# Optimization experiments

Measured on AMD Instinct MI355X. Metric: run time of the kernel, lower is better.

Reference implementation:

```python
import jax, jax.numpy as jnp
import numpy as np

B, T, C, H = 4, 2048, 512, 8
HS = C // H  # head_size = 64
EPS = 1e-5


def layernorm(x, g, b):
    mu = jnp.mean(x, axis=-1, keepdims=True)
    var = jnp.mean(jnp.square(x - mu), axis=-1, keepdims=True)
    return (x - mu) * jax.lax.rsqrt(var + EPS) * g + b


def setup_inputs() -> dict:
    key = jax.random.key(0)
    ks = jax.random.split(key, 12)
    s_attn = 1.0 / np.sqrt(C)
    s_ff1 = 1.0 / np.sqrt(C)
    s_ff2 = 1.0 / np.sqrt(4 * C)
    return {
        "x": jax.random.normal(ks[0], (B, T, C), jnp.float32),
        "wq": jax.random.normal(ks[1], (H, C, HS), jnp.float32) * s_attn,
        "wk": jax.random.normal(ks[2], (H, C, HS), jnp.float32) * s_attn,
        "wv": jax.random.normal(ks[3], (H, C, HS), jnp.float32) * s_attn,
        "w1": jax.random.normal(ks[4], (C, 4 * C), jnp.float32) * s_ff1,
        "b1": jnp.zeros((4 * C,), jnp.float32),
        "w2": jax.random.normal(ks[5], (4 * C, C), jnp.float32) * s_ff2,
        "b2": jnp.zeros((C,), jnp.float32),
        "ln1_g": jnp.ones((C,), jnp.float32),
        "ln1_b": jnp.zeros((C,), jnp.float32),
        "ln2_g": jnp.ones((C,), jnp.float32),
        "ln2_b": jnp.zeros((C,), jnp.float32),
    }


def reference(x, wq, wk, wv, w1, b1, w2, b2, ln1_g, ln1_b, ln2_g, ln2_b):
    # pre-LN multi-head causal self-attention
    h = layernorm(x, ln1_g, ln1_b)                       # [B,T,C]
    q = jnp.einsum("btc,hcd->bhtd", h, wq)
    k = jnp.einsum("btc,hcd->bhtd", h, wk)
    v = jnp.einsum("btc,hcd->bhtd", h, wv)
    # NOTE: source scales by full embed dim C, not head_size
    scores = jnp.einsum("bhtd,bhsd->bhts", q, k) * (C ** -0.5)  # [B,H,T,T]
    causal = jnp.tril(jnp.ones((T, T), bool))
    scores = jnp.where(causal, scores, -jnp.inf)
    att = jax.nn.softmax(scores, axis=-1)
    out = jnp.einsum("bhts,bhsd->bhtd", att, v)          # [B,H,T,HS]
    out = out.transpose(0, 2, 1, 3).reshape(B, T, C)     # concat heads
    x = x + out
    # FFN with residual
    h2 = layernorm(x, ln2_g, ln2_b)
    ff = jax.nn.relu(h2 @ w1 + b1) @ w2 + b2
    return x + ff
```

## Files before the change

kernel.cpp:

```cpp
#include <hip/hip_runtime.h>

typedef unsigned short ushort_t;
typedef __attribute__((ext_vector_type(8))) short short8;
typedef __attribute__((ext_vector_type(4))) float floatx4;

#define B_  4
#define T_  2048
#define C_  512
#define H_  8
#define HS_ 64
#define M_  (B_*T_)
#define SCALE2 0.06376140168547404f

__device__ __forceinline__ float b2f(ushort_t u) {
  union { unsigned int i; float f; } w; w.i = ((unsigned int)u) << 16; return w.f;
}
__device__ __forceinline__ ushort_t f2b(float f) {
  union { float f; unsigned int i; } w; w.f = f;
  unsigned int x = w.i;
  return (ushort_t)((x + 0x7fffu + ((x >> 16) & 1u)) >> 16);
}
__device__ __forceinline__ unsigned int cvtpk(float a, float b) {
  unsigned int r;
  asm("v_cvt_pk_bf16_f32 %0, %1, %2" : "=v"(r) : "v"(a), "v"(b));
  return r;
}
__device__ __forceinline__ void gl_lds16(const ushort_t* g, ushort_t* l) {
  __builtin_amdgcn_global_load_lds((const unsigned int*)g, (unsigned int*)l, 16, 0, 0);
}

__global__ __launch_bounds__(256) void transpose_all(const float* __restrict__ wq,
                                                     const float* __restrict__ wk,
                                                     const float* __restrict__ wv,
                                                     const float* __restrict__ w1,
                                                     const float* __restrict__ w2,
                                                     ushort_t* __restrict__ qkvt,
                                                     ushort_t* __restrict__ w1t,
                                                     ushort_t* __restrict__ w2t) {
  __shared__ ushort_t t[32][33];
  int idx = blockIdx.x;
  const float* in; ushort_t* out; int K, N, bx, by, z = 0;
  float scl = (idx < 256) ? SCALE2 : 1.0f;
  if (idx < 768) {
    int seg = idx >> 8, li = idx & 255;
    in = seg == 0 ? wq : (seg == 1 ? wk : wv);
    out = qkvt + (size_t)seg * 262144;
    K = 512; N = 64;
    z = li >> 5; li &= 31;
    bx = li & 1; by = li >> 1;
  } else if (idx < 1792) {
    int li = idx - 768;
    in = w1; out = w1t; K = 512; N = 2048;
    bx = li & 63; by = li >> 6;
  } else {
    int li = idx - 1792;
    in = w2; out = w2t; K = 2048; N = 512;
    bx = li & 15; by = li >> 4;
  }
  size_t zoff = (size_t)z * K * N;
  int n0 = bx * 32, k0 = by * 32;
  int tx = threadIdx.x & 31, ty = threadIdx.x >> 5;
#pragma unroll
  for (int i = 0; i < 4; i++)
    t[ty + 8 * i][tx] = f2b(in[zoff + (size_t)(k0 + ty + 8 * i) * N + n0 + tx] * scl);
  __syncthreads();
#pragma unroll
  for (int i = 0; i < 4; i++)
    out[zoff + (size_t)(n0 + ty + 8 * i) * K + k0 + tx] = t[tx][ty + 8 * i];
}

__global__ __launch_bounds__(256) void ln_k(const float* __restrict__ X,
                                            const float* __restrict__ g,
                                            const float* __restrict__ bb,
                                            ushort_t* __restrict__ Y) {
  int wave = threadIdx.x >> 6, lane = threadIdx.x & 63;
  size_t row = (size_t)blockIdx.x * 4 + wave;
  float v[8], s = 0.f, s2 = 0.f;
#pragma unroll
  for (int i = 0; i < 8; i++) {
    float x = X[row * C_ + lane + 64 * i];
    v[i] = x; s += x; s2 += x * x;
  }
#pragma unroll
  for (int off = 32; off >= 1; off >>= 1) {
    s += __shfl_xor(s, off); s2 += __shfl_xor(s2, off);
  }
  float mu = s * (1.0f / C_);
  float var = s2 * (1.0f / C_) - mu * mu;
  float rs = rsqrtf(var + 1e-5f);
  ushort_t* yr = Y + row * C_;
#pragma unroll
  for (int i = 0; i < 8; i++) {
    int c = lane + 64 * i;
    yr[c] = f2b((v[i] - mu) * rs * g[c] + bb[c]);
  }
}

__global__ __launch_bounds__(256) void gemm_bt128(const ushort_t* __restrict__ A,
                                                  const ushort_t* __restrict__ Bt,
                                                  ushort_t* __restrict__ Out,
                                                  int K, int ldOut,
                                                  const float* __restrict__ bias,
                                                  int relu) {
  __shared__ __align__(16) ushort_t As[128 * 64];
  __shared__ __align__(16) ushort_t Bs[128 * 64];
  const int tid = threadIdx.x;
  const int lane = tid & 63, wave = tid >> 6;
  const long row0 = (long)blockIdx.x * 128;
  const long col0 = (long)blockIdx.y * 128;
  const int srow = wave * 32 + (lane >> 3);
  const int scol = (((lane & 7) ^ ((lane >> 3) & 7))) * 8;
  const ushort_t* Ab = A + (size_t)(row0 + srow) * K + scol;
  const ushort_t* Bb = Bt + (size_t)(col0 + srow) * K + scol;
  const int wm = (wave >> 1) * 64, wn = (wave & 1) * 64;
  const int fq = lane >> 4, fl = lane & 15;
  floatx4 acc[4][4] = {};

  for (int k0 = 0; k0 < K; k0 += 64) {
    __syncthreads();
#pragma unroll
    for (int i = 0; i < 4; i++) {
      gl_lds16(Ab + (size_t)(i * 8) * K + k0, &As[(wave * 32 + i * 8) * 64]);
      gl_lds16(Bb + (size_t)(i * 8) * K + k0, &Bs[(wave * 32 + i * 8) * 64]);
    }
    __syncthreads();
#pragma unroll
    for (int ks = 0; ks < 2; ks++) {
      short8 af[4], bf[4];
      const int sl = ((ks * 4 + fq) ^ (fl & 7)) * 8;
#pragma unroll
      for (int i = 0; i < 4; i++) {
        af[i] = *(const short8*)&As[(wm + i * 16 + fl) * 64 + sl];
        bf[i] = *(const short8*)&Bs[(wn + i * 16 + fl) * 64 + sl];
      }
#pragma unroll
      for (int fi = 0; fi < 4; fi++)
#pragma unroll
        for (int fj = 0; fj < 4; fj++)
          acc[fi][fj] = __builtin_amdgcn_mfma_f32_16x16x32_bf16(af[fi], bf[fj], acc[fi][fj], 0, 0, 0);
    }
  }
#pragma unroll
  for (int fi = 0; fi < 4; fi++)
#pragma unroll
    for (int fj = 0; fj < 4; fj++) {
      long gcol = col0 + wn + fj * 16 + fl;
      float bv = bias ? bias[gcol] : 0.0f;
#pragma unroll
      for (int r = 0; r < 4; r++) {
        long grow = row0 + wm + fi * 16 + fq * 4 + r;
        float v = acc[fi][fj][r] + bv;
        if (relu) v = fmaxf(v, 0.0f);
        Out[(size_t)grow * ldOut + gcol] = f2b(v);
      }
    }
}

__global__ __launch_bounds__(256) void gemm_bt128_f32(const ushort_t* __restrict__ A,
                                                      const ushort_t* __restrict__ Bt,
                                                      float* __restrict__ Out,
                                                      int K, int ldOut,
                                                      const float* __restrict__ bias,
                                                      const float* __restrict__ residual) {
  __shared__ __align__(16) ushort_t As[128 * 64];
  __shared__ __align__(16) ushort_t Bs[128 * 64];
  const int tid = threadIdx.x;
  const int lane = tid & 63, wave = tid >> 6;
  const long row0 = (long)blockIdx.x * 128;
  const long col0 = (long)blockIdx.y * 128;
  const int srow = wave * 32 + (lane >> 3);
  const int scol = (((lane & 7) ^ ((lane >> 3) & 7))) * 8;
  const ushort_t* Ab = A + (size_t)(row0 + srow) * K + scol;
  const ushort_t* Bb = Bt + (size_t)(col0 + srow) * K + scol;
  const int wm = (wave >> 1) * 64, wn = (wave & 1) * 64;
  const int fq = lane >> 4, fl = lane & 15;
  floatx4 acc[4][4] = {};

  for (int k0 = 0; k0 < K; k0 += 64) {
    __syncthreads();
#pragma unroll
    for (int i = 0; i < 4; i++) {
      gl_lds16(Ab + (size_t)(i * 8) * K + k0, &As[(wave * 32 + i * 8) * 64]);
      gl_lds16(Bb + (size_t)(i * 8) * K + k0, &Bs[(wave * 32 + i * 8) * 64]);
    }
    __syncthreads();
#pragma unroll
    for (int ks = 0; ks < 2; ks++) {
      short8 af[4], bf[4];
      const int sl = ((ks * 4 + fq) ^ (fl & 7)) * 8;
#pragma unroll
      for (int i = 0; i < 4; i++) {
        af[i] = *(const short8*)&As[(wm + i * 16 + fl) * 64 + sl];
        bf[i] = *(const short8*)&Bs[(wn + i * 16 + fl) * 64 + sl];
      }
#pragma unroll
      for (int fi = 0; fi < 4; fi++)
#pragma unroll
        for (int fj = 0; fj < 4; fj++)
          acc[fi][fj] = __builtin_amdgcn_mfma_f32_16x16x32_bf16(af[fi], bf[fj], acc[fi][fj], 0, 0, 0);
    }
  }
#pragma unroll
  for (int fi = 0; fi < 4; fi++)
#pragma unroll
    for (int fj = 0; fj < 4; fj++) {
      long gcol = col0 + wn + fj * 16 + fl;
      float bv = bias[gcol];
#pragma unroll
      for (int r = 0; r < 4; r++) {
        long grow = row0 + wm + fi * 16 + fq * 4 + r;
        size_t oi = (size_t)grow * ldOut + gcol;
        Out[oi] = acc[fi][fj][r] + bv + residual[oi];
      }
    }
}

__global__ __launch_bounds__(256) void gemm_bt64(const ushort_t* __restrict__ A,
                                                 const ushort_t* __restrict__ Bt,
                                                 float* __restrict__ Out,
                                                 int K, int ldOut,
                                                 const float* __restrict__ bias,
                                                 const float* __restrict__ residual) {
  __shared__ __align__(16) ushort_t As[64 * 64];
  __shared__ __align__(16) ushort_t Bs[64 * 64];
  const int tid = threadIdx.x;
  const int lane = tid & 63, wave = tid >> 6;
  const long row0 = (long)blockIdx.x * 64;
  const long col0 = (long)blockIdx.y * 64;
  const int srow = wave * 16 + (lane >> 3);
  const int scol = (((lane & 7) ^ ((lane >> 3) & 7))) * 8;
  const ushort_t* Ab = A + (size_t)(row0 + srow) * K + scol;
  const ushort_t* Bb = Bt + (size_t)(col0 + srow) * K + scol;
  const int wm = (wave >> 1) * 32, wn = (wave & 1) * 32;
  const int fq = lane >> 4, fl = lane & 15;
  floatx4 acc[2][2] = {};

  for (int k0 = 0; k0 < K; k0 += 64) {
    __syncthreads();
#pragma unroll
    for (int i = 0; i < 2; i++) {
      gl_lds16(Ab + (size_t)(i * 8) * K + k0, &As[(wave * 16 + i * 8) * 64]);
      gl_lds16(Bb + (size_t)(i * 8) * K + k0, &Bs[(wave * 16 + i * 8) * 64]);
    }
    __syncthreads();
#pragma unroll
    for (int ks = 0; ks < 2; ks++) {
      short8 af[2], bf[2];
      const int sl = ((ks * 4 + fq) ^ (fl & 7)) * 8;
#pragma unroll
      for (int i = 0; i < 2; i++) {
        af[i] = *(const short8*)&As[(wm + i * 16 + fl) * 64 + sl];
        bf[i] = *(const short8*)&Bs[(wn + i * 16 + fl) * 64 + sl];
      }
#pragma unroll
      for (int fi = 0; fi < 2; fi++)
#pragma unroll
        for (int fj = 0; fj < 2; fj++)
          acc[fi][fj] = __builtin_amdgcn_mfma_f32_16x16x32_bf16(af[fi], bf[fj], acc[fi][fj], 0, 0, 0);
    }
  }
#pragma unroll
  for (int fi = 0; fi < 2; fi++)
#pragma unroll
    for (int fj = 0; fj < 2; fj++) {
      long gcol = col0 + wn + fj * 16 + fl;
      float bv = bias[gcol];
#pragma unroll
      for (int r = 0; r < 4; r++) {
        long grow = row0 + wm + fi * 16 + fq * 4 + r;
        size_t oi = (size_t)grow * ldOut + gcol;
        Out[oi] = acc[fi][fj][r] + bv + residual[oi];
      }
    }
}

__global__ __launch_bounds__(256) void flash_attn(const ushort_t* __restrict__ QKV,
                                                  const float* __restrict__ X,
                                                  float* __restrict__ X1) {
  __shared__ __align__(16) ushort_t kt[2][64 * 72];
  __shared__ __align__(16) ushort_t vt[2][64 * 72];
  const int tid = threadIdx.x;
  const int lane = tid & 63, wave = tid >> 6;
  const int fq = lane >> 4, fl = lane & 15;
  const int g = blockIdx.x >> 5;
  const int tile = g < 16 ? 31 - g : g - 16;
  const int bh = blockIdx.x & 31;
  const int h = bh & 7, b = bh >> 3;
  const int hoff = h * HS_;
  const int q0 = tile * 64;
  const int LD = 3 * C_;
  const int nst = tile + 1;
  const int qg = q0 + wave * 16 + fl;

  short8 qf0, qf1;
  {
    const ushort_t* qp = QKV + (size_t)((size_t)b * T_ + q0 + wave * 16 + fl) * LD + hoff + fq * 8;
    qf0 = *(const short8*)(qp);
    qf1 = *(const short8*)(qp + 32);
  }
  short8 of;
  {
    short ob = (fl == 0) ? (short)0x3F80 : (short)0;
#pragma unroll
    for (int i = 0; i < 8; i++) of[i] = ob;
  }
  floatx4 oacc[4] = {};
  floatx4 lacc = {};

  const int role = tid >> 7;
  const int t2 = tid & 127;
  const int sr4 = (t2 >> 3) * 4;
  const int d0 = (t2 & 7) * 8;
  const ushort_t* sbase = QKV + (size_t)((size_t)b * T_ + sr4) * LD + hoff +
                          (role ? C_ : 2 * C_);

  const int addrA = ((2 * (fq & 1)) * 16 + fl) * 4;
  const int addrB = addrA + 64;
  const bool lowq = fq < 2;

  short8 r0 = *(const short8*)(sbase + d0);
  short8 r1 = *(const short8*)(sbase + LD + d0);
  short8 r2 = *(const short8*)(sbase + 2 * LD + d0);
  short8 r3 = *(const short8*)(sbase + 3 * LD + d0);
  if (role) {
    *(short8*)&kt[0][sr4 * 72 + d0] = r0;
    *(short8*)&kt[0][(sr4 + 1) * 72 + d0] = r1;
    *(short8*)&kt[0][(sr4 + 2) * 72 + d0] = r2;
    *(short8*)&kt[0][(sr4 + 3) * 72 + d0] = r3;
  } else {
#pragma unroll
    for (int i = 0; i < 8; i++) {
      int d = d0 + i;
      int scol = sr4 ^ (8 * (d >> 3));
      unsigned int pkA = ((unsigned int)(ushort_t)r0[i]) |
                         (((unsigned int)(ushort_t)r1[i]) << 16);
      unsigned int pkB = ((unsigned int)(ushort_t)r2[i]) |
                         (((unsigned int)(ushort_t)r3[i]) << 16);
      *(unsigned int*)&vt[0][d * 72 + scol] = pkA;
      *(unsigned int*)&vt[0][d * 72 + scol + 2] = pkB;
    }
  }
  {
    const ushort_t* sp = sbase + (size_t)64 * LD;
    r0 = *(const short8*)(sp + d0);
    r1 = *(const short8*)(sp + LD + d0);
    r2 = *(const short8*)(sp + 2 * LD + d0);
    r3 = *(const short8*)(sp + 3 * LD + d0);
  }

  for (int st = 0; st < nst; st++) {
    __syncthreads();
    const int cur = st & 1;
    if (st + 1 < nst) {
      const int nb = cur ^ 1;
      if (role) {
        *(short8*)&kt[nb][sr4 * 72 + d0] = r0;
        *(short8*)&kt[nb][(sr4 + 1) * 72 + d0] = r1;
        *(short8*)&kt[nb][(sr4 + 2) * 72 + d0] = r2;
        *(short8*)&kt[nb][(sr4 + 3) * 72 + d0] = r3;
      } else {
#pragma unroll
        for (int i = 0; i < 8; i++) {
          int d = d0 + i;
          int scol = sr4 ^ (8 * (d >> 3));
          unsigned int pkA = ((unsigned int)(ushort_t)r0[i]) |
                             (((unsigned int)(ushort_t)r1[i]) << 16);
          unsigned int pkB = ((unsigned int)(ushort_t)r2[i]) |
                             (((unsigned int)(ushort_t)r3[i]) << 16);
          *(unsigned int*)&vt[nb][d * 72 + scol] = pkA;
          *(unsigned int*)&vt[nb][d * 72 + scol + 2] = pkB;
        }
      }
      if (st + 2 < nst) {
        const ushort_t* sp = sbase + (size_t)(st + 2) * 64 * LD;
        r0 = *(const short8*)(sp + d0);
        r1 = *(const short8*)(sp + LD + d0);
        r2 = *(const short8*)(sp + 2 * LD + d0);
        r3 = *(const short8*)(sp + 3 * LD + d0);
      }
    }

    {
      const int s0 = st * 64;
      floatx4 sacc[4] = {};
#pragma unroll
      for (int fn = 0; fn < 4; fn++) {
        short8 kf0 = *(const short8*)&kt[cur][(fn * 16 + fl) * 72 + fq * 8];
        short8 kf1 = *(const short8*)&kt[cur][(fn * 16 + fl) * 72 + 32 + fq * 8];
        sacc[fn] = __builtin_amdgcn_mfma_f32_16x16x32_bf16(kf0, qf0, sacc[fn], 0, 0, 0);
        sacc[fn] = __builtin_amdgcn_mfma_f32_16x16x32_bf16(kf1, qf1, sacc[fn], 0, 0, 0);
      }
      const bool diag = (st == tile);
      unsigned int xc[4][2];
#pragma unroll
      for (int fn = 0; fn < 4; fn++) {
        float p[4];
#pragma unroll
        for (int r = 0; r < 4; r++) {
          float pv = exp2f(sacc[fn][r]);
          if (diag && (s0 + fn * 16 + fq * 4 + r) > qg) pv = 0.0f;
          p[r] = pv;
        }
        xc[fn][0] = cvtpk(p[0], p[1]);
        xc[fn][1] = cvtpk(p[2], p[3]);
      }
      union U8 { unsigned int u[4]; short8 s8; } pu[2];
#pragma unroll
      for (int o = 0; o < 2; o++)
#pragma unroll
        for (int t = 0; t < 4; t++) {
          int ad = (t >> 1) ? addrB : addrA;
          int lo = __builtin_amdgcn_ds_bpermute(ad, (int)xc[2 * o][t & 1]);
          int hi = __builtin_amdgcn_ds_bpermute(ad, (int)xc[2 * o + 1][t & 1]);
          pu[o].u[t] = lowq ? (unsigned int)lo : (unsigned int)hi;
        }
      short8 pf0 = pu[0].s8, pf1 = pu[1].s8;
#pragma unroll
      for (int fn = 0; fn < 4; fn++) {
        int drow = fn * 16 + fl;
        int sw = 8 * (drow >> 3);
        short8 vf0 = *(const short8*)&vt[cur][drow * 72 + ((fq * 8) ^ sw)];
        short8 vf1 = *(const short8*)&vt[cur][drow * 72 + ((32 + fq * 8) ^ sw)];
        oacc[fn] = __builtin_amdgcn_mfma_f32_16x16x32_bf16(pf0, vf0, oacc[fn], 0, 0, 0);
        oacc[fn] = __builtin_amdgcn_mfma_f32_16x16x32_bf16(pf1, vf1, oacc[fn], 0, 0, 0);
      }
      lacc = __builtin_amdgcn_mfma_f32_16x16x32_bf16(pf0, of, lacc, 0, 0, 0);
      lacc = __builtin_amdgcn_mfma_f32_16x16x32_bf16(pf1, of, lacc, 0, 0, 0);
    }
  }
#pragma unroll
  for (int r = 0; r < 4; r++) {
    float lr = __shfl(lacc[r], lane & 48);
    float inv = 1.0f / lr;
    int qgr = q0 + wave * 16 + fq * 4 + r;
#pragma unroll
    for (int fn = 0; fn < 4; fn++) {
      int d = fn * 16 + fl;
      size_t oi = ((size_t)b * T_ + qgr) * C_ + hoff + d;
      X1[oi] = oacc[fn][r] * inv + X[oi];
    }
  }
}

extern "C" void kernel_launch(void* const* d_in, const int* in_sizes, int n_in,
                              void* d_out, int out_size, void* d_ws, size_t ws_size,
                              hipStream_t stream) {
  const float* x  = (const float*)d_in[0];
  const float* wq = (const float*)d_in[1];
  const float* wk = (const float*)d_in[2];
  const float* wv = (const float*)d_in[3];
  const float* w1 = (const float*)d_in[4];
  const float* b1 = (const float*)d_in[5];
  const float* w2 = (const float*)d_in[6];
  const float* b2 = (const float*)d_in[7];
  const float* ln1g = (const float*)d_in[8];
  const float* ln1b = (const float*)d_in[9];
  const float* ln2g = (const float*)d_in[10];
  const float* ln2b = (const float*)d_in[11];
  ushort_t* ws = (ushort_t*)d_ws;

  const size_t SZ = (size_t)M_ * C_;
  ushort_t* qkvt = ws;
  ushort_t* w1t  = qkvt + 786432;
  ushort_t* w2t  = w1t + 1048576;
  ushort_t* qkv  = w2t + 1048576;
  ushort_t* h2   = qkv;
  ushort_t* ff1  = qkv + SZ;
  ushort_t* h    = (ushort_t*)d_out;
  float* x1      = (float*)d_out;
  float* outf    = (float*)d_out;

  const size_t need_unsplit = (2883584 + 5 * SZ) * sizeof(ushort_t);

  transpose_all<<<2816, 256, 0, stream>>>(wq, wk, wv, w1, w2, qkvt, w1t, w2t);
  ln_k<<<M_ / 4, 256, 0, stream>>>(x, ln1g, ln1b, h);
  gemm_bt128<<<dim3(64, 12), 256, 0, stream>>>(h, qkvt, qkv, 512, 1536, nullptr, 0);
  flash_attn<<<B_ * H_ * (T_ / 64), 256, 0, stream>>>(qkv, x, x1);
  ln_k<<<M_ / 4, 256, 0, stream>>>(x1, ln2g, ln2b, h2);
  if (ws_size >= need_unsplit) {
    gemm_bt128<<<dim3(64, 16), 256, 0, stream>>>(h2, w1t, ff1, 512, 2048, b1, 1);
    gemm_bt128_f32<<<dim3(64, 4), 256, 0, stream>>>(ff1, w2t, outf, 2048, 512,
                                                    b2, x1);
  } else {
    for (int p = 0; p < 2; p++) {
      const size_t roff = (size_t)p * 4096;
      gemm_bt128<<<dim3(32, 16), 256, 0, stream>>>(h2 + roff * C_, w1t, ff1,
                                                   512, 2048, b1, 1);
      gemm_bt64<<<dim3(64, 8), 256, 0, stream>>>(ff1, w2t, outf + roff * C_,
                                                 2048, 512, b2, x1 + roff * C_);
    }
  }
}
```

Measured before the change: 239.7 us.

## Double-buffer FFN2 GEMM LDS tiles and use 512-thread blocks

Replaces the FFN second GEMM kernel with a version that double-buffers the A/B LDS tiles, issuing the global-to-LDS loads for the next K step before computing the current one, so each iteration needs one barrier instead of two. The block grows to 8 waves, each computing a 64x32 sub-tile instead of 64x64, which halves the accumulator registers per wave and adds latency-hiding parallelism on a grid of only 256 blocks. The cost is twice the LDS per block (64 KB), which can limit blocks per CU. K and ldOut are now hardcoded.

```diff
diff --git a/kernel.cpp b/kernel.cpp
--- a/kernel.cpp
+++ b/kernel.cpp
@@ -156,54 +156,67 @@
     }
 }
 
-__global__ __launch_bounds__(256) void gemm_bt128_f32(const ushort_t* __restrict__ A,
-                                                      const ushort_t* __restrict__ Bt,
-                                                      float* __restrict__ Out,
-                                                      int K, int ldOut,
-                                                      const float* __restrict__ bias,
-                                                      const float* __restrict__ residual) {
-  __shared__ __align__(16) ushort_t As[128 * 64];
-  __shared__ __align__(16) ushort_t Bs[128 * 64];
+__global__ __launch_bounds__(512) void gemm_ffn2(const ushort_t* __restrict__ A,
+                                                 const ushort_t* __restrict__ Bt,
+                                                 float* __restrict__ Out,
+                                                 const float* __restrict__ bias,
+                                                 const float* __restrict__ residual) {
+  const int K = 2048, ldOut = 512;
+  __shared__ __align__(16) ushort_t As[2][128 * 64];
+  __shared__ __align__(16) ushort_t Bs[2][128 * 64];
   const int tid = threadIdx.x;
   const int lane = tid & 63, wave = tid >> 6;
   const long row0 = (long)blockIdx.x * 128;
   const long col0 = (long)blockIdx.y * 128;
-  const int srow = wave * 32 + (lane >> 3);
+  const int srow = wave * 16 + (lane >> 3);
   const int scol = (((lane & 7) ^ ((lane >> 3) & 7))) * 8;
   const ushort_t* Ab = A + (size_t)(row0 + srow) * K + scol;
   const ushort_t* Bb = Bt + (size_t)(col0 + srow) * K + scol;
-  const int wm = (wave >> 1) * 64, wn = (wave & 1) * 64;
+  const int wm = (wave >> 2) * 64, wn = (wave & 3) * 32;
   const int fq = lane >> 4, fl = lane & 15;
-  floatx4 acc[4][4] = {};
-
+  floatx4 acc[4][2] = {};
+
+#pragma unroll
+  for (int i = 0; i < 2; i++) {
+    gl_lds16(Ab + (size_t)(i * 8) * K, &As[0][(wave * 16 + i * 8) * 64]);
+    gl_lds16(Bb + (size_t)(i * 8) * K, &Bs[0][(wave * 16 + i * 8) * 64]);
+  }
+  __syncthreads();
+
+  int cur = 0;
   for (int k0 = 0; k0 < K; k0 += 64) {
+    const int nk = k0 + 64;
+    if (nk < K) {
+      const int nb = cur ^ 1;
+#pragma unroll
+      for (int i = 0; i < 2; i++) {
+        gl_lds16(Ab + (size_t)(i * 8) * K + nk, &As[nb][(wave * 16 + i * 8) * 64]);
+        gl_lds16(Bb + (size_t)(i * 8) * K + nk, &Bs[nb][(wave * 16 + i * 8) * 64]);
+      }
+    }
+#pragma unroll
+    for (int ks = 0; ks < 2; ks++) {
+      short8 af[4], bf[2];
+      const int sl = ((ks * 4 + fq) ^ (fl & 7)) * 8;
+#pragma unroll
+      for (int i = 0; i < 4; i++)
+        af[i] = *(const short8*)&As[cur][(wm + i * 16 + fl) * 64 + sl];
+#pragma unroll
+      for (int j = 0; j < 2; j++)
+        bf[j] = *(const short8*)&Bs[cur][(wn + j * 16 + fl) * 64 + sl];
+#pragma unroll
+      for (int fi = 0; fi < 4; fi++)
+#pragma unroll
+        for (int fj = 0; fj < 2; fj++)
+          acc[fi][fj] = __builtin_amdgcn_mfma_f32_16x16x32_bf16(af[fi], bf[fj], acc[fi][fj], 0, 0, 0);
+    }
     __syncthreads();
-#pragma unroll
-    for (int i = 0; i < 4; i++) {
-      gl_lds16(Ab + (size_t)(i * 8) * K + k0, &As[(wave * 32 + i * 8) * 64]);
-      gl_lds16(Bb + (size_t)(i * 8) * K + k0, &Bs[(wave * 32 + i * 8) * 64]);
-    }
-    __syncthreads();
-#pragma unroll
-    for (int ks = 0; ks < 2; ks++) {
-      short8 af[4], bf[4];
-      const int sl = ((ks * 4 + fq) ^ (fl & 7)) * 8;
-#pragma unroll
-      for (int i = 0; i < 4; i++) {
-        af[i] = *(const short8*)&As[(wm + i * 16 + fl) * 64 + sl];
-        bf[i] = *(const short8*)&Bs[(wn + i * 16 + fl) * 64 + sl];
-      }
-#pragma unroll
-      for (int fi = 0; fi < 4; fi++)
-#pragma unroll
-        for (int fj = 0; fj < 4; fj++)
-          acc[fi][fj] = __builtin_amdgcn_mfma_f32_16x16x32_bf16(af[fi], bf[fj], acc[fi][fj], 0, 0, 0);
-    }
+    cur ^= 1;
   }
 #pragma unroll
   for (int fi = 0; fi < 4; fi++)
 #pragma unroll
-    for (int fj = 0; fj < 4; fj++) {
+    for (int fj = 0; fj < 2; fj++) {
       long gcol = col0 + wn + fj * 16 + fl;
       float bv = bias[gcol];
 #pragma unroll
@@ -479,8 +492,7 @@
   ln_k<<<M_ / 4, 256, 0, stream>>>(x1, ln2g, ln2b, h2);
   if (ws_size >= need_unsplit) {
     gemm_bt128<<<dim3(64, 16), 256, 0, stream>>>(h2, w1t, ff1, 512, 2048, b1, 1);
-    gemm_bt128_f32<<<dim3(64, 4), 256, 0, stream>>>(ff1, w2t, outf, 2048, 512,
-                                                    b2, x1);
+    gemm_ffn2<<<dim3(64, 4), 512, 0, stream>>>(ff1, w2t, outf, b2, x1);
   } else {
     for (int p = 0; p < 2; p++) {
       const size_t roff = (size_t)p * 4096;
```

Result: faster. 229.9 us (-4.1%).
